# Kernel optimization log

Measured on AMD Instinct MI355X. Metric: run time of the kernel, lower is better.

Reference implementation:

```python
import jax, jax.numpy as jnp
import numpy as np

T, S, B, D, H, F, E = 1024, 1024, 4, 1024, 16, 4096, 8
HD = D // H
N = T * B                      # tokens entering MoE
CAP = 2 * N // E               # top-2 capacity per expert


def setup_inputs() -> dict:
    key = jax.random.key(0)
    ks = jax.random.split(key, 16)
    sc = 0.02
    rn = lambda k, shp, s=sc: jax.random.normal(k, shp, jnp.float32) * s
    return {
        "tgt": jax.random.normal(ks[0], (T, B, D), jnp.float32),
        "memory": jax.random.normal(ks[1], (S, B, D), jnp.float32),
        "sa_in_w": rn(ks[2], (3 * D, D)), "sa_in_b": jnp.zeros((3 * D,), jnp.float32),
        "sa_out_w": rn(ks[3], (D, D)), "sa_out_b": jnp.zeros((D,), jnp.float32),
        "ca_in_w": rn(ks[4], (3 * D, D)), "ca_in_b": jnp.zeros((3 * D,), jnp.float32),
        "ca_out_w": rn(ks[5], (D, D)), "ca_out_b": jnp.zeros((D,), jnp.float32),
        "ln1_g": jnp.ones((D,), jnp.float32), "ln1_b": jnp.zeros((D,), jnp.float32),
        "ln2_g": jnp.ones((D,), jnp.float32), "ln2_b": jnp.zeros((D,), jnp.float32),
        "ln3_g": jnp.ones((D,), jnp.float32), "ln3_b": jnp.zeros((D,), jnp.float32),
        "wg": rn(ks[6], (D, E)),
        "w1": rn(ks[7], (E, D, F)), "b1": jnp.zeros((E, F), jnp.float32),
        "w2": rn(ks[8], (E, F, D)), "b2": jnp.zeros((E, D), jnp.float32),
    }


def layer_norm(x, g, b, eps=1e-5):
    mu = jnp.mean(x, axis=-1, keepdims=True)
    var = jnp.var(x, axis=-1, keepdims=True)
    return (x - mu) * jax.lax.rsqrt(var + eps) * g + b


def mha(q_in, k_in, v_in, in_w, in_b, out_w, out_b):
    # q_in: [Tq,B,D], k_in/v_in: [Tk,B,D]; torch MultiheadAttention math (eval)
    wq, wk, wv = jnp.split(in_w, 3, axis=0)
    bq, bk, bv = jnp.split(in_b, 3)
    def heads(x, w, bias):
        y = x @ w.T + bias                       # [Tx,B,D]
        return y.reshape(x.shape[0], B, H, HD).transpose(1, 2, 0, 3)  # [B,H,Tx,hd]
    q, k, v = heads(q_in, wq, bq), heads(k_in, wk, bk), heads(v_in, wv, bv)
    scores = jnp.einsum('bhtd,bhsd->bhts', q, k) / np.sqrt(HD)
    attn = jax.nn.softmax(scores, axis=-1)
    o = jnp.einsum('bhts,bhsd->bhtd', attn, v)   # [B,H,Tq,hd]
    o = o.transpose(2, 0, 1, 3).reshape(q_in.shape[0], B, D)
    return o @ out_w.T + out_b


def moe_top2(x, wg, w1, b1, w2, b2):
    # x: [N,D]. Top-2 gating with capacity dispatch + grouped expert FFN.
    logits = x @ wg                               # [N,E]
    gates = jax.nn.softmax(logits, axis=-1)
    idx1 = jnp.argmax(gates, axis=-1)             # [N]
    m1 = jax.nn.one_hot(idx1, E, dtype=x.dtype)   # [N,E]
    gates_wo1 = jnp.where(m1 > 0, -jnp.inf, logits)
    idx2 = jnp.argmax(gates_wo1, axis=-1)
    m2 = jax.nn.one_hot(idx2, E, dtype=x.dtype)
    ar = jnp.arange(N)
    g1 = gates[ar, idx1]
    g2 = gates[ar, idx2]
    denom = g1 + g2 + 1e-9
    g1, g2 = g1 / denom, g2 / denom
    # positions within each expert buffer (first-come-first-serve, top1 before top2)
    pos1 = jnp.cumsum(m1, axis=0)[ar, idx1] - 1
    counts1 = jnp.sum(m1, axis=0)                 # [E]
    pos2 = jnp.cumsum(m2, axis=0)[ar, idx2] - 1 + counts1[idx2]
    keep1 = (pos1 < CAP).astype(x.dtype)
    keep2 = (pos2 < CAP).astype(x.dtype)
    p1 = jnp.clip(pos1, 0, CAP - 1).astype(jnp.int32)
    p2 = jnp.clip(pos2, 0, CAP - 1).astype(jnp.int32)
    buf = jnp.zeros((E, CAP, D), x.dtype)
    buf = buf.at[idx1, p1].add(x * keep1[:, None])
    buf = buf.at[idx2, p2].add(x * keep2[:, None])
    # grouped expert FFN: [E,CAP,D] -> [E,CAP,F] -> [E,CAP,D]
    h = jax.nn.relu(jnp.einsum('ecd,edf->ecf', buf, w1) + b1[:, None, :])
    eo = jnp.einsum('ecf,efd->ecd', h, w2) + b2[:, None, :]
    out = eo[idx1, p1] * (g1 * keep1)[:, None] + eo[idx2, p2] * (g2 * keep2)[:, None]
    return out


def reference(tgt, memory, sa_in_w, sa_in_b, sa_out_w, sa_out_b,
              ca_in_w, ca_in_b, ca_out_w, ca_out_b,
              ln1_g, ln1_b, ln2_g, ln2_b, ln3_g, ln3_b,
              wg, w1, b1, w2, b2):
    t2 = mha(tgt, tgt, tgt, sa_in_w, sa_in_b, sa_out_w, sa_out_b)
    x = layer_norm(tgt + t2, ln1_g, ln1_b)
    t2 = mha(x, memory, memory, ca_in_w, ca_in_b, ca_out_w, ca_out_b)
    x = layer_norm(x + t2, ln2_g, ln2_b)
    m = moe_top2(x.reshape(N, D), wg, w1, b1, w2, b2).reshape(T, B, D)
    x = layer_norm(x + m, ln3_g, ln3_b)
    return x
```

## Files before the change

### kernel.cpp

```cpp
#include <hip/hip_runtime.h>
#include <hip/hip_bf16.h>


typedef __bf16 bf16;
typedef __bf16 bf16x2 __attribute__((ext_vector_type(2)));
typedef __bf16 bf16x4 __attribute__((ext_vector_type(4)));
typedef __bf16 bf16x8 __attribute__((ext_vector_type(8)));
typedef float  f32x4  __attribute__((ext_vector_type(4)));

static_assert(sizeof(bf16) == 2, "bf16 size");

#define CAP_ 1024

#define GLOAD16(g, l)                                                  \
  __builtin_amdgcn_global_load_lds(                                    \
      (const __attribute__((address_space(1))) unsigned int*)(g),      \
      (__attribute__((address_space(3))) unsigned int*)(l), 16, 0, 0)

#define BAR() do { asm volatile("" ::: "memory"); __builtin_amdgcn_s_barrier(); asm volatile("" ::: "memory"); } while (0)

static const long OFF_WSAIN  = 0L;
static const long OFF_WSAOUT = 6291456L;
static const long OFF_WCAIN  = 8388608L;
static const long OFF_WCAOUT = 14680064L;
static const long OFF_BTGT   = 16777216L;
static const long OFF_BMEM   = 25165824L;
static const long OFF_QKV    = 33554432L;
static const long OFF_EO1    = 33554432L;
static const long OFF_KVCA   = OFF_QKV + 8388608L;
static const long OFF_VT     = 58720256L;
static const long OFF_AO     = 67108864L;
static const long OFF_PROJ   = 75497472L;
static const long OFF_X1     = 92274688L;
static const long OFF_X2     = 109051904L;
static const long OFF_SCORES = 125829120L;
static const long OFF_H      = OFF_SCORES + 67108864L;
static const long OFF_GATE   = 260046848L;
static const long OFF_E1   = OFF_GATE;
static const long OFF_E2   = OFF_GATE + 16384L;
static const long OFF_G1   = OFF_GATE + 32768L;
static const long OFF_G2   = OFF_GATE + 49152L;
static const long OFF_D1   = OFF_GATE + 65536L;
static const long OFF_D2   = OFF_GATE + 81920L;
static const long OFF_S1   = OFF_GATE + 98304L;
static const long OFF_S2   = OFF_GATE + 114688L;
static const long OFF_P2T  = OFF_GATE + 131072L;

__device__ __forceinline__ int xcd_swz(int bid, int nwg) {
  int q = nwg >> 3, r = nwg & 7;
  int xcd = bid & 7, idx = bid >> 3;
  return (xcd < r ? xcd * (q + 1) : r * (q + 1) + (xcd - r) * q) + idx;
}

__global__ __launch_bounds__(256) void k_cvt6(
    const float* __restrict__ s0, const float* __restrict__ s1,
    const float* __restrict__ s2, const float* __restrict__ s3,
    const float* __restrict__ s4, const float* __restrict__ s5,
    bf16* __restrict__ d0, bf16* __restrict__ d1, bf16* __restrict__ d2,
    bf16* __restrict__ d3, bf16* __restrict__ d4, bf16* __restrict__ d5) {
  long b = blockIdx.x;
  const float* s; bf16* d; long off;
  if (b < 3072)       { s = s0; d = d0; off = b; }
  else if (b < 4096)  { s = s1; d = d1; off = b - 3072; }
  else if (b < 7168)  { s = s2; d = d2; off = b - 4096; }
  else if (b < 8192)  { s = s3; d = d3; off = b - 7168; }
  else if (b < 12288) { s = s4; d = d4; off = b - 8192; }
  else                { s = s5; d = d5; off = b - 12288; }
  long i = off * 256 + threadIdx.x;
  float4 v = ((const float4*)s)[i];
  bf16x4 o = {(bf16)v.x, (bf16)v.y, (bf16)v.z, (bf16)v.w};
  ((bf16x4*)d)[i] = o;
}

__global__ __launch_bounds__(256) void k_zero16(float4* __restrict__ p, long n) {
  long i = (long)blockIdx.x * 256 + threadIdx.x;
  if (i < n) p[i] = make_float4(0.f, 0.f, 0.f, 0.f);
}

__global__ __launch_bounds__(256) void k_transpose_f32_bf16(const float* __restrict__ in,
                                                            bf16* __restrict__ out, int R, int C) {
  __shared__ float t[64][70];
  int z = blockIdx.z;
  long r0 = (long)blockIdx.y * 64, c0 = (long)blockIdx.x * 64;
  const float* ib = in + (long)z * R * C;
  bf16* ob = out + (long)z * R * C;
  int x = threadIdx.x, y = threadIdx.y;
  #pragma unroll
  for (int j = 0; j < 4; j++) {
    int sr = y + j * 16;
    float4 v = *(const float4*)&ib[(r0 + sr) * C + c0 + x * 4];
    t[sr][x * 4 + 0] = v.x; t[sr][x * 4 + 1] = v.y;
    t[sr][x * 4 + 2] = v.z; t[sr][x * 4 + 3] = v.w;
  }
  __syncthreads();
  #pragma unroll
  for (int j = 0; j < 4; j++) {
    int sc = y + j * 16;
    #pragma unroll
    for (int i = 0; i < 2; i++) {
      int sr = x * 2 + i * 32;
      bf16x2 o = {(bf16)t[sr][sc], (bf16)t[sr + 1][sc]};
      *(bf16x2*)&ob[(c0 + sc) * R + r0 + sr] = o;
    }
  }
}

__global__ __launch_bounds__(256) void k_extract_vt(const bf16* __restrict__ in,
                                                    bf16* __restrict__ out, long rs, long sb) {
  __shared__ bf16 t[64][66];
  int z = blockIdx.z;
  long r0 = (long)blockIdx.y * 64;
  const bf16* ib = in + (long)(z >> 4) * sb + (long)(z & 15) * 64;
  bf16* ob = out + (long)z * 64 * 1024;
  int x = threadIdx.x, y = threadIdx.y;
  #pragma unroll
  for (int i = y; i < 64; i += 4) t[i][x] = ib[(r0 + i) * rs + x];
  __syncthreads();
  #pragma unroll
  for (int i = y; i < 64; i += 4) ob[(long)i * 1024 + r0 + x] = t[x][i];
}

template <int BM, int BN, int WM, int WN, bool RELU, typename OutT>
__global__ __launch_bounds__(256) void k_gemm_nt(
    const bf16* __restrict__ A, const bf16* __restrict__ Bp,
    OutT* __restrict__ C, const float* __restrict__ bias,
    int K, long lda, long ldb, long ldc, float alpha, int zdiv,
    long sA1, long sA0, long sB1, long sB0, long sC1, long sC0,
    long sBias1, long sBias0) {
  constexpr int BK = 32;
  constexpr int WTM = BM / WM, WTN = BN / WN, MR = WTM / 16, NR = WTN / 16;
  constexpr int AISS = BM * BK / 2048;
  constexpr int BISS = BN * BK / 2048;
  __shared__ bf16 sa[BM * BK];
  __shared__ bf16 sb[BN * BK];
  const int nwg = gridDim.x * gridDim.y * gridDim.z;
  const int bid = blockIdx.x + gridDim.x * (blockIdx.y + gridDim.y * blockIdx.z);
  const int lid = xcd_swz(bid, nwg);
  const int bx = lid % gridDim.x;
  const int rem = lid / gridDim.x;
  const int by = rem % gridDim.y;
  const int z = rem / gridDim.y;
  const int zh = z / zdiv, zl = z - zh * zdiv;
  const bf16* Ab = A + zh * sA1 + zl * sA0 + (long)by * BM * lda;
  const bf16* Bb = Bp + zh * sB1 + zl * sB0 + (long)bx * BN * ldb;
  const int tid = threadIdx.x, lane = tid & 63, wid = tid >> 6;
  const int wm = wid / WN, wn = wid % WN;

  const int srow = tid >> 2;
  const int scol = (tid & 3) * 8;
  const bf16* aptr[AISS];
  bf16* aldst[AISS];
  #pragma unroll
  for (int i = 0; i < AISS; i++) {
    aptr[i] = Ab + (long)(srow + i * 64) * lda + scol;
    aldst[i] = &sa[i * 2048 + (wid << 9)];
  }
  const bf16* bptr[BISS];
  bf16* bldst[BISS];
  #pragma unroll
  for (int i = 0; i < BISS; i++) {
    bptr[i] = Bb + (long)(srow + i * 64) * ldb + scol;
    bldst[i] = &sb[i * 2048 + (wid << 9)];
  }

  f32x4 acc[MR][NR] = {};
  const int rA = wm * WTM + (lane & 15);
  const int rB = wn * WTN + (lane & 15);
  const int kk = (lane >> 4) * 8;

  for (int k0 = 0; k0 < K; k0 += BK) {
    #pragma unroll
    for (int i = 0; i < AISS; i++) GLOAD16(aptr[i] + k0, aldst[i]);
    #pragma unroll
    for (int i = 0; i < BISS; i++) GLOAD16(bptr[i] + k0, bldst[i]);
    __syncthreads();
    bf16x8 af[MR], bfr[NR];
    #pragma unroll
    for (int mi = 0; mi < MR; mi++) af[mi] = *(const bf16x8*)&sa[(rA + mi * 16) * BK + kk];
    #pragma unroll
    for (int ni = 0; ni < NR; ni++) bfr[ni] = *(const bf16x8*)&sb[(rB + ni * 16) * BK + kk];
    #pragma unroll
    for (int mi = 0; mi < MR; mi++)
      #pragma unroll
      for (int ni = 0; ni < NR; ni++)
        acc[mi][ni] = __builtin_amdgcn_mfma_f32_16x16x32_bf16(af[mi], bfr[ni], acc[mi][ni], 0, 0, 0);
    __syncthreads();
  }
  OutT* Cb = C + zh * sC1 + zl * sC0;
  const float* biasb = bias ? (bias + zh * sBias1 + zl * sBias0) : nullptr;
  const long rowBase = (long)by * BM + wm * WTM + ((lane >> 4) * 4);
  const long colBase = (long)bx * BN + wn * WTN + (lane & 15);
  #pragma unroll
  for (int mi = 0; mi < MR; mi++) {
    #pragma unroll
    for (int ni = 0; ni < NR; ni++) {
      long col = colBase + ni * 16;
      float bv = biasb ? biasb[col] : 0.f;
      #pragma unroll
      for (int r = 0; r < 4; r++) {
        long row = rowBase + mi * 16 + r;
        float v = acc[mi][ni][r] * alpha + bv;
        if (RELU) v = fmaxf(v, 0.f);
        Cb[row * ldc + col] = (OutT)v;
      }
    }
  }
}

template <bool RELU, typename OutT>
__global__ __launch_bounds__(512, 2) void k_gemm8p(
    const bf16* __restrict__ A, const bf16* __restrict__ Bp,
    OutT* __restrict__ C, const float* __restrict__ bias,
    int K, long lda, long ldb, long ldc, int zdiv,
    long sA1, long sA0, long sB1, long sB0, long sC1, long sC0, long sBias1) {
  __shared__ bf16 smem[65536];
  const int nwg = gridDim.x * gridDim.y * gridDim.z;
  const int bid = blockIdx.x + gridDim.x * (blockIdx.y + gridDim.y * blockIdx.z);
  const int lid = xcd_swz(bid, nwg);
  const int bx = lid % gridDim.x;
  const int rem = lid / gridDim.x;
  const int by = rem % gridDim.y;
  const int z = rem / gridDim.y;
  const int zh = z / zdiv, zl = z - zh * zdiv;
  const bf16* Ab = A + zh * sA1 + zl * sA0 + (long)by * 256 * lda;
  const bf16* Bb = Bp + zh * sB1 + zl * sB0 + (long)bx * 256 * ldb;
  const int tid = threadIdx.x, lane = tid & 63, wid = tid >> 6;
  const int wm = wid >> 2, wn = wid & 3;
  const int lane15 = lane & 15, grp = lane >> 4;
  const int s_r = (wid << 3) + (lane >> 3);
  const int s_k = ((lane & 7) ^ (lane >> 3)) << 3;
  const int ldst = wid << 9;
  const int in0 = (grp << 4) ^ ((lane & 7) << 4);
  const int in1 = (64 | (grp << 4)) ^ ((lane & 7) << 4);

  const int NT = K >> 6;
  f32x4 acc[8][4] = {};
  bf16x8 a[4][2], b[2][2][2];

  const bf16* pA[4];
  const bf16* pB[4];
  #pragma unroll
  for (int q = 0; q < 4; q++) {
    pA[q] = Ab + (long)((q << 6) + s_r) * lda + s_k;
    pB[q] = Bb + (long)((q << 6) + s_r) * ldb + s_k;
  }

  auto loadA = [&](int mh, int cb) {
    #pragma unroll
    for (int mi2 = 0; mi2 < 4; mi2++) {
      int r = wm * 128 + mh * 64 + mi2 * 16 + lane15;
      a[mi2][0] = *(const bf16x8*)&smem[cb + (r << 6) + (in0 >> 1)];
      a[mi2][1] = *(const bf16x8*)&smem[cb + (r << 6) + (in1 >> 1)];
    }
  };
  auto loadB = [&](int nh, int cb) {
    #pragma unroll
    for (int ni2 = 0; ni2 < 2; ni2++) {
      int c = wn * 64 + nh * 32 + ni2 * 16 + lane15;
      b[nh][ni2][0] = *(const bf16x8*)&smem[cb + 16384 + (c << 6) + (in0 >> 1)];
      b[nh][ni2][1] = *(const bf16x8*)&smem[cb + 16384 + (c << 6) + (in1 >> 1)];
    }
  };
  auto mfmaQ = [&](int mh, int nh) {
    __builtin_amdgcn_s_setprio(1);
    #pragma unroll
    for (int ks = 0; ks < 2; ks++)
      #pragma unroll
      for (int mi2 = 0; mi2 < 4; mi2++)
        #pragma unroll
        for (int ni2 = 0; ni2 < 2; ni2++)
          acc[mh * 4 + mi2][nh * 2 + ni2] = __builtin_amdgcn_mfma_f32_16x16x32_bf16(
              a[mi2][ks], b[nh][ni2][ks], acc[mh * 4 + mi2][nh * 2 + ni2], 0, 0, 0);
    __builtin_amdgcn_s_setprio(0);
  };

  #pragma unroll
  for (int q = 0; q < 4; q++) {
    GLOAD16(pA[q], &smem[(q << 12) + ldst]);
    GLOAD16(pB[q], &smem[16384 + (q << 12) + ldst]);
  }
  #pragma unroll
  for (int q = 0; q < 4; q++) {
    GLOAD16(pA[q] + 64, &smem[32768 + (q << 12) + ldst]);
    GLOAD16(pB[q] + 64, &smem[32768 + 16384 + (q << 12) + ldst]);
  }
  asm volatile("s_waitcnt vmcnt(8)" ::: "memory");
  BAR();

  for (int t = 0; t < NT; t++) {
    const int cb = (t & 1) << 15;
    const bool dostage = (t + 2) < NT;
    loadA(0, cb); loadB(0, cb);
    BAR(); mfmaQ(0, 0); BAR();
    loadB(1, cb);
    if (dostage) {
      GLOAD16(pA[0] + 128, &smem[cb + ldst]);
      GLOAD16(pA[2] + 128, &smem[cb + (2 << 12) + ldst]);
    }
    BAR(); mfmaQ(0, 1); BAR();
    loadA(1, cb);
    if (dostage) {
      GLOAD16(pB[0] + 128, &smem[cb + 16384 + ldst]);
      GLOAD16(pB[1] + 128, &smem[cb + 16384 + (1 << 12) + ldst]);
    }
    BAR(); mfmaQ(1, 1); BAR();
    if (dostage) {
      GLOAD16(pA[1] + 128, &smem[cb + (1 << 12) + ldst]);
      GLOAD16(pA[3] + 128, &smem[cb + (3 << 12) + ldst]);
      GLOAD16(pB[2] + 128, &smem[cb + 16384 + (2 << 12) + ldst]);
      GLOAD16(pB[3] + 128, &smem[cb + 16384 + (3 << 12) + ldst]);
      asm volatile("s_waitcnt vmcnt(8)" ::: "memory");
    } else if (t + 1 < NT) {
      asm volatile("s_waitcnt vmcnt(0)" ::: "memory");
    }
    BAR(); mfmaQ(1, 0); BAR();
    #pragma unroll
    for (int q = 0; q < 4; q++) { pA[q] += 64; pB[q] += 64; }
  }

  float* eb = (float*)smem;
  constexpr int EPS = 264;
  const float* biasb = bias ? (bias + zh * sBias1) : nullptr;
  float bv[4];
  #pragma unroll
  for (int ni = 0; ni < 4; ni++)
    bv[ni] = biasb ? biasb[(long)bx * 256 + wn * 64 + ni * 16 + lane15] : 0.f;
  OutT* Cb = C + zh * sC1 + zl * sC0;
  const int err = tid >> 4;
  const int ecc = (tid & 15) << 4;
  const long grB = (long)by * 256 + (err < 16 ? err : 112 + err);
  const long gcB = (long)bx * 256 + ecc;
  const int wrow = wm * 16 + grp * 4;
  const int wcol = wn * 64 + lane15;
  #pragma unroll
  for (int mi = 0; mi < 8; mi++) {
    BAR();
    #pragma unroll
    for (int ni = 0; ni < 4; ni++) {
      #pragma unroll
      for (int r = 0; r < 4; r++) {
        float v = acc[mi][ni][r] + bv[ni];
        if (RELU) v = fmaxf(v, 0.f);
        eb[(wrow + r) * EPS + wcol + ni * 16] = v;
      }
    }
    BAR();
    float4 vv[4];
    #pragma unroll
    for (int j = 0; j < 4; j++)
      vv[j] = *(const float4*)&eb[err * EPS + ecc + j * 4];
    long grow = grB + mi * 16;
    if constexpr (sizeof(OutT) == 2) {
      bf16x8 o0 = {(bf16)vv[0].x, (bf16)vv[0].y, (bf16)vv[0].z, (bf16)vv[0].w,
                   (bf16)vv[1].x, (bf16)vv[1].y, (bf16)vv[1].z, (bf16)vv[1].w};
      bf16x8 o1 = {(bf16)vv[2].x, (bf16)vv[2].y, (bf16)vv[2].z, (bf16)vv[2].w,
                   (bf16)vv[3].x, (bf16)vv[3].y, (bf16)vv[3].z, (bf16)vv[3].w};
      *(bf16x8*)&Cb[grow * ldc + gcB] = o0;
      *(bf16x8*)&Cb[grow * ldc + gcB + 8] = o1;
    } else {
      #pragma unroll
      for (int j = 0; j < 4; j++)
        *(float4*)&Cb[grow * ldc + gcB + j * 4] = vv[j];
    }
  }
}

__global__ __launch_bounds__(256) void k_flash(
    const bf16* __restrict__ q, const bf16* __restrict__ kk,
    const bf16* __restrict__ vt, bf16* __restrict__ ao,
    long qrs, long krs) {
  __shared__ bf16 kt[2][2048];
  __shared__ bf16 vtt[2][2048];
  __shared__ bf16 p_lds[4][32 * 72];
  const int nwg = gridDim.x * gridDim.y;
  const int bid = blockIdx.x + gridDim.x * blockIdx.y;
  const int lid = xcd_swz(bid, nwg);
  const int qt = lid & 7;
  const int bh = lid >> 3;
  const int b = bh >> 4, h = bh & 15;
  const int tid = threadIdx.x, lane = tid & 63, wid = tid >> 6;
  const int colLane = lane & 15, grp = lane >> 4;
  const bf16* qb = q + (qrs >> 2) * b + h * 64;
  const bf16* kb = kk + (krs >> 2) * b + h * 64;
  const bf16* vb = vt + (long)bh * 65536;

  bf16x8 qf[2][2];
  const int qrow0 = qt * 128 + wid * 32 + colLane;
  #pragma unroll
  for (int mi = 0; mi < 2; mi++)
    #pragma unroll
    for (int ks = 0; ks < 2; ks++)
      qf[mi][ks] = *(const bf16x8*)&qb[(long)(qrow0 + mi * 16) * qrs + ks * 32 + grp * 8];

  const int srow = tid >> 2;
  const int scol = (tid & 3) * 8;

  f32x4 oacc[2][4] = {};
  float m_[2][4], l_[2][4];
  #pragma unroll
  for (int mi = 0; mi < 2; mi++)
    #pragma unroll
    for (int r = 0; r < 4; r++) { m_[mi][r] = -INFINITY; l_[mi][r] = 0.f; }
  bf16* pl = &p_lds[wid][0];

  for (int s0 = 0; s0 < 1024; s0 += 64) {
    GLOAD16(&kb[(long)(s0 + srow) * krs + scol], &kt[0][wid << 9]);
    GLOAD16(&kb[(long)(s0 + srow) * krs + 32 + scol], &kt[1][wid << 9]);
    GLOAD16(&vb[(long)srow * 1024 + s0 + scol], &vtt[0][wid << 9]);
    GLOAD16(&vb[(long)srow * 1024 + s0 + 32 + scol], &vtt[1][wid << 9]);
    __syncthreads();

    f32x4 sacc[2][4] = {};
    bf16x8 kf[4][2];
    #pragma unroll
    for (int ni = 0; ni < 4; ni++)
      #pragma unroll
      for (int ks = 0; ks < 2; ks++)
        kf[ni][ks] = *(const bf16x8*)&kt[ks][(colLane + ni * 16) * 32 + grp * 8];
    #pragma unroll
    for (int ks = 0; ks < 2; ks++)
      #pragma unroll
      for (int mi = 0; mi < 2; mi++)
        #pragma unroll
        for (int ni = 0; ni < 4; ni++)
          sacc[mi][ni] = __builtin_amdgcn_mfma_f32_16x16x32_bf16(qf[mi][ks], kf[ni][ks], sacc[mi][ni], 0, 0, 0);

    float mnew[2][4], sc[2][4], psum[2][4];
    #pragma unroll
    for (int mi = 0; mi < 2; mi++)
      #pragma unroll
      for (int r = 0; r < 4; r++) {
        float vx = fmaxf(fmaxf(sacc[mi][0][r], sacc[mi][1][r]),
                         fmaxf(sacc[mi][2][r], sacc[mi][3][r])) * 0.125f;
        #pragma unroll
        for (int o = 1; o < 16; o <<= 1) vx = fmaxf(vx, __shfl_xor(vx, o));
        float mn = fmaxf(m_[mi][r], vx);
        sc[mi][r] = __expf(m_[mi][r] - mn);
        m_[mi][r] = mn; mnew[mi][r] = mn;
        l_[mi][r] *= sc[mi][r];
        psum[mi][r] = 0.f;
      }
    #pragma unroll
    for (int mi = 0; mi < 2; mi++)
      #pragma unroll
      for (int ni = 0; ni < 4; ni++)
        #pragma unroll
        for (int r = 0; r < 4; r++)
          oacc[mi][ni][r] *= sc[mi][r];
    #pragma unroll
    for (int mi = 0; mi < 2; mi++)
      #pragma unroll
      for (int ni = 0; ni < 4; ni++)
        #pragma unroll
        for (int r = 0; r < 4; r++) {
          float p = __expf(sacc[mi][ni][r] * 0.125f - mnew[mi][r]);
          psum[mi][r] += p;
          pl[(mi * 16 + grp * 4 + r) * 72 + ni * 16 + colLane] = (bf16)p;
        }
    #pragma unroll
    for (int mi = 0; mi < 2; mi++)
      #pragma unroll
      for (int r = 0; r < 4; r++) {
        float ps = psum[mi][r];
        #pragma unroll
        for (int o = 1; o < 16; o <<= 1) ps += __shfl_xor(ps, o);
        l_[mi][r] += ps;
      }

    bf16x8 pa[2][2], vf[4][2];
    #pragma unroll
    for (int mi = 0; mi < 2; mi++)
      #pragma unroll
      for (int ks = 0; ks < 2; ks++)
        pa[mi][ks] = *(const bf16x8*)&pl[(colLane + mi * 16) * 72 + ks * 32 + grp * 8];
    #pragma unroll
    for (int ni = 0; ni < 4; ni++)
      #pragma unroll
      for (int ks = 0; ks < 2; ks++)
        vf[ni][ks] = *(const bf16x8*)&vtt[ks][(colLane + ni * 16) * 32 + grp * 8];
    #pragma unroll
    for (int ks = 0; ks < 2; ks++)
      #pragma unroll
      for (int mi = 0; mi < 2; mi++)
        #pragma unroll
        for (int ni = 0; ni < 4; ni++)
          oacc[mi][ni] = __builtin_amdgcn_mfma_f32_16x16x32_bf16(pa[mi][ks], vf[ni][ks], oacc[mi][ni], 0, 0, 0);
    __syncthreads();
  }

  #pragma unroll
  for (int mi = 0; mi < 2; mi++)
    #pragma unroll
    for (int r = 0; r < 4; r++) {
      float inv = 1.f / l_[mi][r];
      int t = qt * 128 + wid * 32 + mi * 16 + grp * 4 + r;
      long n = (long)t * 4 + b;
      #pragma unroll
      for (int ni = 0; ni < 4; ni++)
        ao[n * 1024 + h * 64 + ni * 16 + colLane] = (bf16)(oacc[mi][ni][r] * inv);
    }
}

__global__ __launch_bounds__(256) void k_add_ln(const float* __restrict__ a, const float* __restrict__ b,
                                                const float* __restrict__ g, const float* __restrict__ be,
                                                float* __restrict__ out, bf16* __restrict__ outb) {
  long row = blockIdx.x;
  int tid = threadIdx.x;
  const float* pa = a + row * 1024;
  const float* pb = b + row * 1024;
  float v[4];
  float s = 0.f, sq = 0.f;
  #pragma unroll
  for (int i = 0; i < 4; i++) {
    int c = tid + i * 256;
    float x = pa[c] + pb[c];
    v[i] = x; s += x; sq += x * x;
  }
  #pragma unroll
  for (int o = 32; o; o >>= 1) { s += __shfl_xor(s, o); sq += __shfl_xor(sq, o); }
  __shared__ float r1[4], r2[4];
  int wid = tid >> 6;
  if ((tid & 63) == 0) { r1[wid] = s; r2[wid] = sq; }
  __syncthreads();
  s = r1[0] + r1[1] + r1[2] + r1[3];
  sq = r2[0] + r2[1] + r2[2] + r2[3];
  float mu = s * (1.f / 1024.f);
  float var = sq * (1.f / 1024.f) - mu * mu;
  float rstd = rsqrtf(var + 1e-5f);
  #pragma unroll
  for (int i = 0; i < 4; i++) {
    int c = tid + i * 256;
    float y = (v[i] - mu) * rstd * g[c] + be[c];
    out[row * 1024 + c] = y;
    if (outb) outb[row * 1024 + c] = (bf16)y;
  }
}

__global__ __launch_bounds__(256) void k_gate(const float* __restrict__ x, const float* __restrict__ wg,
                                              int* __restrict__ e1, int* __restrict__ e2,
                                              float* __restrict__ g1, float* __restrict__ g2) {
  int n = blockIdx.x * 4 + (threadIdx.x >> 6);
  int lane = threadIdx.x & 63;
  const float* xr = x + (long)n * 1024;
  float acc[8] = {0.f, 0.f, 0.f, 0.f, 0.f, 0.f, 0.f, 0.f};
  for (int i = 0; i < 16; i++) {
    float xv = xr[i * 64 + lane];
    const float* wr = wg + (long)(i * 64 + lane) * 8;
    #pragma unroll
    for (int e = 0; e < 8; e++) acc[e] += xv * wr[e];
  }
  #pragma unroll
  for (int e = 0; e < 8; e++)
    #pragma unroll
    for (int o = 32; o; o >>= 1) acc[e] += __shfl_xor(acc[e], o);
  if (lane == 0) {
    int i1 = 0; float b1v = acc[0];
    #pragma unroll
    for (int e = 1; e < 8; e++) if (acc[e] > b1v) { b1v = acc[e]; i1 = e; }
    int i2 = -1; float b2v = -INFINITY;
    #pragma unroll
    for (int e = 0; e < 8; e++) if (e != i1 && acc[e] > b2v) { b2v = acc[e]; i2 = e; }
    float den = 0.f;
    #pragma unroll
    for (int e = 0; e < 8; e++) den += __expf(acc[e] - b1v);
    float gg1 = 1.f / den;
    float gg2 = __expf(b2v - b1v) / den;
    float dn = gg1 + gg2 + 1e-9f;
    e1[n] = i1; e2[n] = i2; g1[n] = gg1 / dn; g2[n] = gg2 / dn;
  }
}

__global__ __launch_bounds__(64) void k_positions(const int* __restrict__ e1, const int* __restrict__ e2,
                                                  const float* __restrict__ g1, const float* __restrict__ g2,
                                                  int* __restrict__ d1, int* __restrict__ d2,
                                                  float* __restrict__ s1, float* __restrict__ s2,
                                                  int* __restrict__ p2t) {
  const int lane = threadIdx.x;
  int base1[8] = {0, 0, 0, 0, 0, 0, 0, 0};
  int base2[8] = {0, 0, 0, 0, 0, 0, 0, 0};
  const unsigned long long lt = (1ull << lane) - 1ull;
  int na = e1[lane], nb = e2[lane];
  for (int c = 0; c < 64; c++) {
    int a = na, b = nb;
    if (c < 63) { na = e1[(c + 1) * 64 + lane]; nb = e2[(c + 1) * 64 + lane]; }
    int n = c * 64 + lane;
    int pa = 0, pb = 0;
    #pragma unroll
    for (int e = 0; e < 8; e++) {
      unsigned long long ba = __ballot(a == e);
      unsigned long long bb = __ballot(b == e);
      if (a == e) pa = base1[e] + __popcll(ba & lt);
      if (b == e) pb = base2[e] + __popcll(bb & lt);
      base1[e] += __popcll(ba);
      base2[e] += __popcll(bb);
    }
    d1[n] = a * CAP_ + (pa < CAP_ ? pa : CAP_ - 1);
    s1[n] = (pa < CAP_) ? g1[n] : 0.f;
    p2t[n] = pb;
  }
  __shared__ int c1[8];
  if (lane == 0) {
    c1[0] = base1[0]; c1[1] = base1[1]; c1[2] = base1[2]; c1[3] = base1[3];
    c1[4] = base1[4]; c1[5] = base1[5]; c1[6] = base1[6]; c1[7] = base1[7];
  }
  __syncthreads();
  for (int c = 0; c < 64; c++) {
    int n = c * 64 + lane;
    int b = e2[n];
    int pb = p2t[n] + c1[b];
    d2[n] = b * CAP_ + (pb < CAP_ ? pb : CAP_ - 1);
    s2[n] = (pb < CAP_) ? g2[n] : 0.f;
  }
}

__global__ __launch_bounds__(256) void k_scatter(const float* __restrict__ x, const int* __restrict__ d1,
                                                 const int* __restrict__ d2, const float* __restrict__ s1,
                                                 const float* __restrict__ s2, bf16* __restrict__ buf) {
  int n = blockIdx.x;
  int tid = threadIdx.x;
  const float* xr = x + (long)n * 1024;
  float v[4];
  #pragma unroll
  for (int i = 0; i < 4; i++) v[i] = xr[tid + i * 256];
  if (s1[n] != 0.f) {
    bf16* o = buf + (long)d1[n] * 1024;
    #pragma unroll
    for (int i = 0; i < 4; i++) o[tid + i * 256] = (bf16)v[i];
  }
  if (s2[n] != 0.f) {
    bf16* o = buf + (long)d2[n] * 1024;
    #pragma unroll
    for (int i = 0; i < 4; i++) o[tid + i * 256] = (bf16)v[i];
  }
}

__global__ __launch_bounds__(256) void k_gather_ln(const float* __restrict__ x,
                                                   const float* __restrict__ p0, const float* __restrict__ p1,
                                                   const float* __restrict__ b2,
                                                   const int* __restrict__ d1, const int* __restrict__ d2,
                                                   const float* __restrict__ s1, const float* __restrict__ s2,
                                                   const float* __restrict__ g, const float* __restrict__ be,
                                                   float* __restrict__ out) {
  long n = blockIdx.x;
  int tid = threadIdx.x;
  float a1 = s1[n], a2 = s2[n];
  long i1 = (long)d1[n] * 1024, i2 = (long)d2[n] * 1024;
  long e1b = (long)(d1[n] >> 10) * 1024, e2b = (long)(d2[n] >> 10) * 1024;
  const float* xr = x + n * 1024;
  float v[4];
  float s = 0.f, sq = 0.f;
  #pragma unroll
  for (int i = 0; i < 4; i++) {
    int c = tid + i * 256;
    float r1v = p0[i1 + c] + p1[i1 + c] + b2[e1b + c];
    float r2v = p0[i2 + c] + p1[i2 + c] + b2[e2b + c];
    float y = xr[c] + a1 * r1v + a2 * r2v;
    v[i] = y; s += y; sq += y * y;
  }
  #pragma unroll
  for (int o = 32; o; o >>= 1) { s += __shfl_xor(s, o); sq += __shfl_xor(sq, o); }
  __shared__ float r1[4], r2[4];
  int wid = tid >> 6;
  if ((tid & 63) == 0) { r1[wid] = s; r2[wid] = sq; }
  __syncthreads();
  s = r1[0] + r1[1] + r1[2] + r1[3];
  sq = r2[0] + r2[1] + r2[2] + r2[3];
  float mu = s * (1.f / 1024.f);
  float var = sq * (1.f / 1024.f) - mu * mu;
  float rstd = rsqrtf(var + 1e-5f);
  #pragma unroll
  for (int i = 0; i < 4; i++) {
    int c = tid + i * 256;
    out[n * 1024 + c] = (v[i] - mu) * rstd * g[c] + be[c];
  }
}

extern "C" void kernel_launch(void* const* d_in, const int* in_sizes, int n_in,
                              void* d_out, int out_size, void* d_ws, size_t ws_size,
                              hipStream_t stream) {
  const float* tgt      = (const float*)d_in[0];
  const float* memory   = (const float*)d_in[1];
  const float* sa_in_w  = (const float*)d_in[2];
  const float* sa_in_b  = (const float*)d_in[3];
  const float* sa_out_w = (const float*)d_in[4];
  const float* sa_out_b = (const float*)d_in[5];
  const float* ca_in_w  = (const float*)d_in[6];
  const float* ca_in_b  = (const float*)d_in[7];
  const float* ca_out_w = (const float*)d_in[8];
  const float* ca_out_b = (const float*)d_in[9];
  const float* ln1_g    = (const float*)d_in[10];
  const float* ln1_b    = (const float*)d_in[11];
  const float* ln2_g    = (const float*)d_in[12];
  const float* ln2_b    = (const float*)d_in[13];
  const float* ln3_g    = (const float*)d_in[14];
  const float* ln3_b    = (const float*)d_in[15];
  const float* wg       = (const float*)d_in[16];
  const float* w1       = (const float*)d_in[17];
  const float* b1       = (const float*)d_in[18];
  const float* w2       = (const float*)d_in[19];
  const float* b2       = (const float*)d_in[20];

  char* ws = (char*)d_ws;
  auto B16 = [&](long o) { return (bf16*)(ws + o); };
  auto F32 = [&](long o) { return (float*)(ws + o); };
  auto I32 = [&](long o) { return (int*)(ws + o); };

  const dim3 blk256(256), blk512(512), blkT16(16, 16), blkT(64, 4);

  k_cvt6<<<16384, blk256, 0, stream>>>(sa_in_w, sa_out_w, ca_in_w, ca_out_w, tgt, memory,
                                       B16(OFF_WSAIN), B16(OFF_WSAOUT), B16(OFF_WCAIN),
                                       B16(OFF_WCAOUT), B16(OFF_BTGT), B16(OFF_BMEM));

  k_gemm8p<false, bf16><<<dim3(12, 16, 1), blk512, 0, stream>>>(
      B16(OFF_BTGT), B16(OFF_WSAIN), B16(OFF_QKV), sa_in_b,
      1024, 1024, 1024, 3072, 1, 0, 0, 0, 0, 0, 0, 0);
  k_extract_vt<<<dim3(1, 16, 64), blkT, 0, stream>>>(B16(OFF_QKV) + 2048, B16(OFF_VT), 12288, 3072);
  k_flash<<<dim3(8, 64), blk256, 0, stream>>>(
      B16(OFF_QKV), B16(OFF_QKV) + 1024, B16(OFF_VT), B16(OFF_AO), 12288, 12288);
  k_gemm_nt<128, 64, 4, 1, false, float><<<dim3(16, 32, 1), blk256, 0, stream>>>(
      B16(OFF_AO), B16(OFF_WSAOUT), F32(OFF_PROJ), sa_out_b,
      1024, 1024, 1024, 1024, 1.f, 1, 0, 0, 0, 0, 0, 0, 0, 0);
  k_add_ln<<<4096, blk256, 0, stream>>>(tgt, F32(OFF_PROJ), ln1_g, ln1_b, F32(OFF_X1), B16(OFF_BTGT));

  k_gemm_nt<128, 64, 4, 1, false, bf16><<<dim3(16, 32, 1), blk256, 0, stream>>>(
      B16(OFF_BTGT), B16(OFF_WCAIN), B16(OFF_QKV), ca_in_b,
      1024, 1024, 1024, 1024, 1.f, 1, 0, 0, 0, 0, 0, 0, 0, 0);
  k_gemm_nt<128, 64, 4, 1, false, bf16><<<dim3(32, 32, 1), blk256, 0, stream>>>(
      B16(OFF_BMEM), B16(OFF_WCAIN) + 1024L * 1024, B16(OFF_KVCA), ca_in_b + 1024,
      1024, 1024, 1024, 2048, 1.f, 1, 0, 0, 0, 0, 0, 0, 0, 0);
  k_extract_vt<<<dim3(1, 16, 64), blkT, 0, stream>>>(B16(OFF_KVCA) + 1024, B16(OFF_VT), 8192, 2048);
  k_flash<<<dim3(8, 64), blk256, 0, stream>>>(
      B16(OFF_QKV), B16(OFF_KVCA), B16(OFF_VT), B16(OFF_AO), 4096, 8192);
  k_gemm_nt<128, 64, 4, 1, false, float><<<dim3(16, 32, 1), blk256, 0, stream>>>(
      B16(OFF_AO), B16(OFF_WCAOUT), F32(OFF_PROJ), ca_out_b,
      1024, 1024, 1024, 1024, 1.f, 1, 0, 0, 0, 0, 0, 0, 0, 0);
  k_add_ln<<<4096, blk256, 0, stream>>>(F32(OFF_X1), F32(OFF_PROJ), ln2_g, ln2_b, F32(OFF_X2), (bf16*)nullptr);

  k_gate<<<1024, blk256, 0, stream>>>(F32(OFF_X2), wg, I32(OFF_E1), I32(OFF_E2), F32(OFF_G1), F32(OFF_G2));
  k_positions<<<1, 64, 0, stream>>>(I32(OFF_E1), I32(OFF_E2), F32(OFF_G1), F32(OFF_G2),
                                    I32(OFF_D1), I32(OFF_D2), F32(OFF_S1), F32(OFF_S2), I32(OFF_P2T));
  k_zero16<<<4096, blk256, 0, stream>>>((float4*)B16(OFF_QKV), 1048576L);
  k_scatter<<<4096, blk256, 0, stream>>>(F32(OFF_X2), I32(OFF_D1), I32(OFF_D2),
                                         F32(OFF_S1), F32(OFF_S2), B16(OFF_QKV));
  k_transpose_f32_bf16<<<dim3(64, 16, 8), blkT16, 0, stream>>>(w1, B16(OFF_SCORES), 1024, 4096);
  k_gemm8p<true, bf16><<<dim3(16, 4, 8), blk512, 0, stream>>>(
      B16(OFF_QKV), B16(OFF_SCORES), B16(OFF_H), b1,
      1024, 1024, 1024, 4096, 1,
      1048576, 0, 4194304, 0, 4194304, 0, 4096);
  k_transpose_f32_bf16<<<dim3(16, 64, 8), blkT16, 0, stream>>>(w2, B16(OFF_SCORES), 4096, 1024);
  k_gemm8p<false, float><<<dim3(4, 4, 16), blk512, 0, stream>>>(
      B16(OFF_H), B16(OFF_SCORES), F32(OFF_PROJ), nullptr,
      2048, 4096, 4096, 1024, 2,
      4194304, 2048, 4194304, 2048, 1048576, (OFF_EO1 - OFF_PROJ) / 4, 0);
  k_gather_ln<<<4096, blk256, 0, stream>>>(F32(OFF_X2), F32(OFF_PROJ), F32(OFF_EO1), b2,
                                           I32(OFF_D1), I32(OFF_D2),
                                           F32(OFF_S1), F32(OFF_S2), ln3_g, ln3_b, (float*)d_out);

  (void)in_sizes; (void)n_in; (void)out_size; (void)ws_size;
}
```

Before: 641.8 us.

## Parallelize MoE positions, drop buffer zeroing, write bf16 expert partials directly

```diff
diff --git a/kernel.cpp b/kernel.cpp
--- a/kernel.cpp
+++ b/kernel.cpp
@@ -44,7 +44,6 @@
 static const long OFF_D2   = OFF_GATE + 81920L;
 static const long OFF_S1   = OFF_GATE + 98304L;
 static const long OFF_S2   = OFF_GATE + 114688L;
-static const long OFF_P2T  = OFF_GATE + 131072L;
 
 __device__ __forceinline__ int xcd_swz(int bid, int nwg) {
   int q = nwg >> 3, r = nwg & 7;
@@ -70,11 +69,6 @@
   float4 v = ((const float4*)s)[i];
   bf16x4 o = {(bf16)v.x, (bf16)v.y, (bf16)v.z, (bf16)v.w};
   ((bf16x4*)d)[i] = o;
-}
-
-__global__ __launch_bounds__(256) void k_zero16(float4* __restrict__ p, long n) {
-  long i = (long)blockIdx.x * 256 + threadIdx.x;
-  if (i < n) p[i] = make_float4(0.f, 0.f, 0.f, 0.f);
 }
 
 __global__ __launch_bounds__(256) void k_transpose_f32_bf16(const float* __restrict__ in,
@@ -318,49 +312,26 @@
     for (int q = 0; q < 4; q++) { pA[q] += 64; pB[q] += 64; }
   }
 
-  float* eb = (float*)smem;
-  constexpr int EPS = 264;
+  OutT* Cb = C + zh * sC1 + zl * sC0;
   const float* biasb = bias ? (bias + zh * sBias1) : nullptr;
   float bv[4];
   #pragma unroll
   for (int ni = 0; ni < 4; ni++)
     bv[ni] = biasb ? biasb[(long)bx * 256 + wn * 64 + ni * 16 + lane15] : 0.f;
-  OutT* Cb = C + zh * sC1 + zl * sC0;
-  const int err = tid >> 4;
-  const int ecc = (tid & 15) << 4;
-  const long grB = (long)by * 256 + (err < 16 ? err : 112 + err);
-  const long gcB = (long)bx * 256 + ecc;
-  const int wrow = wm * 16 + grp * 4;
-  const int wcol = wn * 64 + lane15;
+  const long rowBase = (long)by * 256 + wm * 128 + grp * 4;
+  const long colBase = (long)bx * 256 + wn * 64 + lane15;
   #pragma unroll
   for (int mi = 0; mi < 8; mi++) {
-    BAR();
     #pragma unroll
     for (int ni = 0; ni < 4; ni++) {
+      long col = colBase + ni * 16;
       #pragma unroll
       for (int r = 0; r < 4; r++) {
+        long row = rowBase + mi * 16 + r;
         float v = acc[mi][ni][r] + bv[ni];
         if (RELU) v = fmaxf(v, 0.f);
-        eb[(wrow + r) * EPS + wcol + ni * 16] = v;
+        Cb[row * ldc + col] = (OutT)v;
       }
-    }
-    BAR();
-    float4 vv[4];
-    #pragma unroll
-    for (int j = 0; j < 4; j++)
-      vv[j] = *(const float4*)&eb[err * EPS + ecc + j * 4];
-    long grow = grB + mi * 16;
-    if constexpr (sizeof(OutT) == 2) {
-      bf16x8 o0 = {(bf16)vv[0].x, (bf16)vv[0].y, (bf16)vv[0].z, (bf16)vv[0].w,
-                   (bf16)vv[1].x, (bf16)vv[1].y, (bf16)vv[1].z, (bf16)vv[1].w};
-      bf16x8 o1 = {(bf16)vv[2].x, (bf16)vv[2].y, (bf16)vv[2].z, (bf16)vv[2].w,
-                   (bf16)vv[3].x, (bf16)vv[3].y, (bf16)vv[3].z, (bf16)vv[3].w};
-      *(bf16x8*)&Cb[grow * ldc + gcB] = o0;
-      *(bf16x8*)&Cb[grow * ldc + gcB + 8] = o1;
-    } else {
-      #pragma unroll
-      for (int j = 0; j < 4; j++)
-        *(float4*)&Cb[grow * ldc + gcB + j * 4] = vv[j];
     }
   }
 }
@@ -570,46 +541,55 @@
   }
 }
 
-__global__ __launch_bounds__(64) void k_positions(const int* __restrict__ e1, const int* __restrict__ e2,
-                                                  const float* __restrict__ g1, const float* __restrict__ g2,
-                                                  int* __restrict__ d1, int* __restrict__ d2,
-                                                  float* __restrict__ s1, float* __restrict__ s2,
-                                                  int* __restrict__ p2t) {
-  const int lane = threadIdx.x;
-  int base1[8] = {0, 0, 0, 0, 0, 0, 0, 0};
-  int base2[8] = {0, 0, 0, 0, 0, 0, 0, 0};
-  const unsigned long long lt = (1ull << lane) - 1ull;
-  int na = e1[lane], nb = e2[lane];
-  for (int c = 0; c < 64; c++) {
-    int a = na, b = nb;
-    if (c < 63) { na = e1[(c + 1) * 64 + lane]; nb = e2[(c + 1) * 64 + lane]; }
-    int n = c * 64 + lane;
-    int pa = 0, pb = 0;
-    #pragma unroll
-    for (int e = 0; e < 8; e++) {
-      unsigned long long ba = __ballot(a == e);
-      unsigned long long bb = __ballot(b == e);
-      if (a == e) pa = base1[e] + __popcll(ba & lt);
-      if (b == e) pb = base2[e] + __popcll(bb & lt);
-      base1[e] += __popcll(ba);
-      base2[e] += __popcll(bb);
-    }
-    d1[n] = a * CAP_ + (pa < CAP_ ? pa : CAP_ - 1);
-    s1[n] = (pa < CAP_) ? g1[n] : 0.f;
-    p2t[n] = pb;
-  }
-  __shared__ int c1[8];
-  if (lane == 0) {
-    c1[0] = base1[0]; c1[1] = base1[1]; c1[2] = base1[2]; c1[3] = base1[3];
-    c1[4] = base1[4]; c1[5] = base1[5]; c1[6] = base1[6]; c1[7] = base1[7];
-  }
+__global__ __launch_bounds__(256) void k_positions(const int* __restrict__ e1, const int* __restrict__ e2,
+                                                   const float* __restrict__ g1, const float* __restrict__ g2,
+                                                   int* __restrict__ d1, int* __restrict__ d2,
+                                                   float* __restrict__ s1, float* __restrict__ s2) {
+  const int e = blockIdx.x;
+  const int tid = threadIdx.x, lane = tid & 63, wid = tid >> 6;
+  __shared__ int wsum[4];
+  int f[16];
+  int cnt = 0;
+  #pragma unroll
+  for (int i = 0; i < 16; i++) { f[i] = (e1[tid * 16 + i] == e) ? 1 : 0; cnt += f[i]; }
+  int inc = cnt;
+  #pragma unroll
+  for (int o = 1; o < 64; o <<= 1) { int v = __shfl_up(inc, o); if (lane >= o) inc += v; }
+  if (lane == 63) wsum[wid] = inc;
   __syncthreads();
-  for (int c = 0; c < 64; c++) {
-    int n = c * 64 + lane;
-    int b = e2[n];
-    int pb = p2t[n] + c1[b];
-    d2[n] = b * CAP_ + (pb < CAP_ ? pb : CAP_ - 1);
-    s2[n] = (pb < CAP_) ? g2[n] : 0.f;
+  int base = inc - cnt;
+  for (int w = 0; w < wid; w++) base += wsum[w];
+  const int total1 = wsum[0] + wsum[1] + wsum[2] + wsum[3];
+  int run = base;
+  #pragma unroll
+  for (int i = 0; i < 16; i++) {
+    int n = tid * 16 + i;
+    if (f[i]) {
+      int p = run++;
+      d1[n] = e * CAP_ + (p < CAP_ ? p : CAP_ - 1);
+      s1[n] = (p < CAP_) ? g1[n] : 0.f;
+    }
+  }
+  cnt = 0;
+  #pragma unroll
+  for (int i = 0; i < 16; i++) { f[i] = (e2[tid * 16 + i] == e) ? 1 : 0; cnt += f[i]; }
+  inc = cnt;
+  #pragma unroll
+  for (int o = 1; o < 64; o <<= 1) { int v = __shfl_up(inc, o); if (lane >= o) inc += v; }
+  __syncthreads();
+  if (lane == 63) wsum[wid] = inc;
+  __syncthreads();
+  base = inc - cnt + total1;
+  for (int w = 0; w < wid; w++) base += wsum[w];
+  run = base;
+  #pragma unroll
+  for (int i = 0; i < 16; i++) {
+    int n = tid * 16 + i;
+    if (f[i]) {
+      int p = run++;
+      d2[n] = e * CAP_ + (p < CAP_ ? p : CAP_ - 1);
+      s2[n] = (p < CAP_) ? g2[n] : 0.f;
+    }
   }
 }
 
@@ -635,7 +615,7 @@
 }
 
 __global__ __launch_bounds__(256) void k_gather_ln(const float* __restrict__ x,
-                                                   const float* __restrict__ p0, const float* __restrict__ p1,
+                                                   const bf16* __restrict__ p0, const bf16* __restrict__ p1,
                                                    const float* __restrict__ b2,
                                                    const int* __restrict__ d1, const int* __restrict__ d2,
                                                    const float* __restrict__ s1, const float* __restrict__ s2,
@@ -652,8 +632,8 @@
   #pragma unroll
   for (int i = 0; i < 4; i++) {
     int c = tid + i * 256;
-    float r1v = p0[i1 + c] + p1[i1 + c] + b2[e1b + c];
-    float r2v = p0[i2 + c] + p1[i2 + c] + b2[e2b + c];
+    float r1v = (float)p0[i1 + c] + (float)p1[i1 + c] + b2[e1b + c];
+    float r2v = (float)p0[i2 + c] + (float)p1[i2 + c] + b2[e2b + c];
     float y = xr[c] + a1 * r1v + a2 * r2v;
     v[i] = y; s += y; sq += y * y;
   }
@@ -737,9 +717,8 @@
   k_add_ln<<<4096, blk256, 0, stream>>>(F32(OFF_X1), F32(OFF_PROJ), ln2_g, ln2_b, F32(OFF_X2), (bf16*)nullptr);
 
   k_gate<<<1024, blk256, 0, stream>>>(F32(OFF_X2), wg, I32(OFF_E1), I32(OFF_E2), F32(OFF_G1), F32(OFF_G2));
-  k_positions<<<1, 64, 0, stream>>>(I32(OFF_E1), I32(OFF_E2), F32(OFF_G1), F32(OFF_G2),
-                                    I32(OFF_D1), I32(OFF_D2), F32(OFF_S1), F32(OFF_S2), I32(OFF_P2T));
-  k_zero16<<<4096, blk256, 0, stream>>>((float4*)B16(OFF_QKV), 1048576L);
+  k_positions<<<8, blk256, 0, stream>>>(I32(OFF_E1), I32(OFF_E2), F32(OFF_G1), F32(OFF_G2),
+                                        I32(OFF_D1), I32(OFF_D2), F32(OFF_S1), F32(OFF_S2));
   k_scatter<<<4096, blk256, 0, stream>>>(F32(OFF_X2), I32(OFF_D1), I32(OFF_D2),
                                          F32(OFF_S1), F32(OFF_S2), B16(OFF_QKV));
   k_transpose_f32_bf16<<<dim3(64, 16, 8), blkT16, 0, stream>>>(w1, B16(OFF_SCORES), 1024, 4096);
@@ -748,11 +727,11 @@
       1024, 1024, 1024, 4096, 1,
       1048576, 0, 4194304, 0, 4194304, 0, 4096);
   k_transpose_f32_bf16<<<dim3(16, 64, 8), blkT16, 0, stream>>>(w2, B16(OFF_SCORES), 4096, 1024);
-  k_gemm8p<false, float><<<dim3(4, 4, 16), blk512, 0, stream>>>(
-      B16(OFF_H), B16(OFF_SCORES), F32(OFF_PROJ), nullptr,
+  k_gemm8p<false, bf16><<<dim3(4, 4, 16), blk512, 0, stream>>>(
+      B16(OFF_H), B16(OFF_SCORES), B16(OFF_PROJ), nullptr,
       2048, 4096, 4096, 1024, 2,
-      4194304, 2048, 4194304, 2048, 1048576, (OFF_EO1 - OFF_PROJ) / 4, 0);
-  k_gather_ln<<<4096, blk256, 0, stream>>>(F32(OFF_X2), F32(OFF_PROJ), F32(OFF_EO1), b2,
+      4194304, 2048, 4194304, 2048, 1048576, (OFF_EO1 - OFF_PROJ) / 2, 0);
+  k_gather_ln<<<4096, blk256, 0, stream>>>(F32(OFF_X2), B16(OFF_PROJ), B16(OFF_EO1), b2,
                                            I32(OFF_D1), I32(OFF_D2),
                                            F32(OFF_S1), F32(OFF_S2), ln3_g, ln3_b, (float*)d_out);
 
```

New measurement: 557.7 us. 1.15x faster.
